# Kernel optimization log

Hardware: AMD Instinct MI355X
Metric: run time of the kernel (lower is better)

## Reference

```python
import jax, jax.numpy as jnp
import numpy as np

D_MODEL = 512
NUM_HEADS = 8


def setup_inputs() -> dict:
    key = jax.random.key(0)
    ks = jax.random.split(key, 12)
    B, S, D = 2, 4096, D_MODEL
    s = 1.0 / np.sqrt(D)
    return {
        "q": jax.random.normal(ks[0], (B, S, D), jnp.float32),
        "k": jax.random.normal(ks[1], (B, S, D), jnp.float32),
        "v": jax.random.normal(ks[2], (B, S, D), jnp.float32),
        "w_q": jax.random.normal(ks[3], (D, D), jnp.float32) * s,
        "b_q": jax.random.normal(ks[4], (D,), jnp.float32) * s,
        "w_k": jax.random.normal(ks[5], (D, D), jnp.float32) * s,
        "b_k": jax.random.normal(ks[6], (D,), jnp.float32) * s,
        "w_v": jax.random.normal(ks[7], (D, D), jnp.float32) * s,
        "b_v": jax.random.normal(ks[8], (D,), jnp.float32) * s,
        "w_o": jax.random.normal(ks[9], (D, D), jnp.float32) * s,
        "b_o": jax.random.normal(ks[10], (D,), jnp.float32) * s,
    }


def _split(x, num_heads):
    B, S, D = x.shape
    return x.reshape(B, S, num_heads, D // num_heads).transpose(0, 2, 1, 3)


def reference(q, k, v, w_q, b_q, w_k, b_k, w_v, b_v, w_o, b_o):
    # Linear projections (torch Linear: x @ W^T + b)
    qp = q @ w_q.T + b_q
    kp = k @ w_k.T + b_k
    vp = v @ w_v.T + b_v
    # split into heads: [B, H, S, d_head]
    qh = _split(qp, NUM_HEADS)
    kh = _split(kp, NUM_HEADS)
    vh = _split(vp, NUM_HEADS)
    d_head = qh.shape[-1]
    # NOTE: original scales by sqrt(d_model of the per-head tensor) == sqrt(d_head)
    score = jnp.einsum("bhqd,bhkd->bhqk", qh, kh) / jnp.sqrt(jnp.float32(d_head))
    attn = jax.nn.softmax(score, axis=-1)  # full [B,H,S,S] materialized, as in source
    out = jnp.einsum("bhqk,bhkd->bhqd", attn, vh)
    # concat heads back to [B, S, D]
    B, H, S, Dh = out.shape
    out = out.transpose(0, 2, 1, 3).reshape(B, S, H * Dh)
    return out @ w_o.T + b_o
```

## Files before the change

### kernel.cpp

```cpp
#include <hip/hip_runtime.h>
#include <math.h>

typedef __bf16 bf16_t;
typedef __bf16 bf16x4_v __attribute__((ext_vector_type(4)));
typedef __bf16 bf16x8_t __attribute__((ext_vector_type(8)));
typedef float f32x4_t __attribute__((ext_vector_type(4)));
typedef unsigned uint2_t __attribute__((ext_vector_type(2)));
typedef unsigned uint4_t __attribute__((ext_vector_type(4)));

#define S_LEN 4096
#define DM 512
#define NH 8
#define DH 64
#define MTOT 8192

#define Q_SCALE 0.1803368801111204f

#define REG   4194304
#define WREG  262144
#define W_OFF (3 * REG)
#define CVT_TOTAL (3 * REG + 4 * WREG)
#define QH_OFF CVT_TOTAL

__device__ inline f32x4_t mfma16(bf16x8_t a, bf16x8_t b, f32x4_t c) {
    return __builtin_amdgcn_mfma_f32_16x16x32_bf16(a, b, c, 0, 0, 0);
}

__device__ inline unsigned pkbf16(float a, float b) {
    unsigned short ra = __builtin_bit_cast(unsigned short, (bf16_t)a);
    unsigned short rb = __builtin_bit_cast(unsigned short, (bf16_t)b);
    return (unsigned)ra | ((unsigned)rb << 16);
}

__device__ inline void async_copy16(const void* g, void* l) {
    __builtin_amdgcn_global_load_lds(
        (const __attribute__((address_space(1))) void*)g,
        (__attribute__((address_space(3))) void*)l, 16, 0, 0);
}

__global__ __launch_bounds__(256) void cvt_all(
    const float* __restrict__ q, const float* __restrict__ k, const float* __restrict__ v,
    const float* __restrict__ wq, const float* __restrict__ wk,
    const float* __restrict__ wv, const float* __restrict__ wo,
    bf16_t* __restrict__ dst)
{
    long gidx = (long)blockIdx.x * 2048 + (long)threadIdx.x * 8;
    const float* src;
    long off = gidx;
    if      (gidx < 1L * REG)          { src = q; }
    else if (gidx < 2L * REG)          { src = k;  off = gidx - 1L * REG; }
    else if (gidx < 3L * REG)          { src = v;  off = gidx - 2L * REG; }
    else if (gidx < W_OFF + 1L * WREG) { src = wq; off = gidx - W_OFF; }
    else if (gidx < W_OFF + 2L * WREG) { src = wk; off = gidx - (W_OFF + 1L * WREG); }
    else if (gidx < W_OFF + 3L * WREG) { src = wv; off = gidx - (W_OFF + 2L * WREG); }
    else                               { src = wo; off = gidx - (W_OFF + 3L * WREG); }
    float4 a = *(const float4*)(src + off);
    float4 b = *(const float4*)(src + off + 4);
    bf16x8_t h;
    h[0] = (bf16_t)a.x; h[1] = (bf16_t)a.y; h[2] = (bf16_t)a.z; h[3] = (bf16_t)a.w;
    h[4] = (bf16_t)b.x; h[5] = (bf16_t)b.y; h[6] = (bf16_t)b.z; h[7] = (bf16_t)b.w;
    *(bf16x8_t*)(dst + gidx) = h;
}

__global__ __launch_bounds__(256) void gemm_qkv(
    const bf16_t* __restrict__ XWb,
    const float* __restrict__ B0, const float* __restrict__ B1, const float* __restrict__ B2,
    bf16_t* __restrict__ dst_base)
{
    const int p = blockIdx.z;
    const bf16_t* __restrict__ X = XWb + (size_t)p * REG;
    const bf16_t* __restrict__ W = XWb + W_OFF + (size_t)p * WREG;
    const float* __restrict__ Bi = (p == 0) ? B0 : ((p == 1) ? B1 : B2);
    bf16_t* __restrict__ dst = dst_base + (size_t)p * REG;

    const int m0 = blockIdx.x * 128;
    const int n0 = blockIdx.y * 128;
    const int tid = threadIdx.x;
    const int lane = tid & 63, wid = tid >> 6;
    const int lm = lane & 15, lg = lane >> 4;
    const int wm = (wid >> 1) * 64, wn = (wid & 1) * 64;

    __shared__ __align__(16) bf16_t As[128 * 64];
    __shared__ __align__(16) bf16_t Bs[128 * 64];

    f32x4_t acc[4][4] = {};

    const int r0 = tid >> 3, c7 = tid & 7;
    const int cA0 = ((lg) ^ (lm & 7)) * 8;
    const int cA1 = ((4 + lg) ^ (lm & 7)) * 8;

    for (int kb = 0; kb < DM / 64; ++kb) {
        const int k0 = kb * 64;
#pragma unroll
        for (int i = 0; i < 4; ++i) {
            int row = i * 32 + r0;
            int ch = c7 ^ (row & 7);
            async_copy16(X + (size_t)(m0 + row) * DM + k0 + ch * 8, (char*)As + (i * 256 + tid) * 16);
            async_copy16(W + (size_t)(n0 + row) * DM + k0 + ch * 8, (char*)Bs + (i * 256 + tid) * 16);
        }
        __syncthreads();
#pragma unroll
        for (int kd = 0; kd < 2; ++kd) {
            const int co = kd ? cA1 : cA0;
            bf16x8_t fa[4], fb[4];
#pragma unroll
            for (int mt = 0; mt < 4; ++mt) {
                fa[mt] = *(const bf16x8_t*)(As + (wm + mt * 16 + lm) * 64 + co);
                fb[mt] = *(const bf16x8_t*)(Bs + (wn + mt * 16 + lm) * 64 + co);
            }
            if (p < 2) {
#pragma unroll
                for (int mt = 0; mt < 4; ++mt)
#pragma unroll
                    for (int nt = 0; nt < 4; ++nt)
                        acc[nt][mt] = mfma16(fb[nt], fa[mt], acc[nt][mt]);
            } else {
#pragma unroll
                for (int mt = 0; mt < 4; ++mt)
#pragma unroll
                    for (int nt = 0; nt < 4; ++nt)
                        acc[mt][nt] = mfma16(fa[mt], fb[nt], acc[mt][nt]);
            }
        }
        __syncthreads();
    }

    if (p == 2) {
#pragma unroll
        for (int nt = 0; nt < 4; ++nt) {
            int col = n0 + wn + nt * 16 + lm;
            float bv = Bi[col];
            int h = (col >> 6) & 7, dc = col & 63;
#pragma unroll
            for (int mt = 0; mt < 4; ++mt) {
                int mrow = m0 + wm + mt * 16 + lg * 4;
                int bb = mrow >> 12, s = mrow & (S_LEN - 1);
                bf16x4_v pk;
#pragma unroll
                for (int r = 0; r < 4; ++r) pk[r] = (bf16_t)(acc[mt][nt][r] + bv);
                *(bf16x4_v*)&dst[(((size_t)(bb * NH + h)) * DH + dc) * S_LEN + s] = pk;
            }
        }
    } else {
        const float scale = (p == 0) ? Q_SCALE : 1.0f;
#pragma unroll
        for (int nt = 0; nt < 4; ++nt) {
            int ncol = n0 + wn + nt * 16 + lg * 4;
            float4 bv4 = *(const float4*)&Bi[ncol];
            int h = (ncol >> 6) & 7, dc = ncol & 63;
#pragma unroll
            for (int mt = 0; mt < 4; ++mt) {
                int m = m0 + wm + mt * 16 + lm;
                int bb = m >> 12, s = m & (S_LEN - 1);
                bf16x4_v pk;
                pk[0] = (bf16_t)((acc[nt][mt][0] + bv4.x) * scale);
                pk[1] = (bf16_t)((acc[nt][mt][1] + bv4.y) * scale);
                pk[2] = (bf16_t)((acc[nt][mt][2] + bv4.z) * scale);
                pk[3] = (bf16_t)((acc[nt][mt][3] + bv4.w) * scale);
                *(bf16x4_v*)&dst[(((size_t)(bb * NH + h)) * S_LEN + s) * DH + dc] = pk;
            }
        }
    }
}

__global__ __launch_bounds__(512, 4) void flash_attn(
    const bf16_t* __restrict__ Qh, const bf16_t* __restrict__ Kh,
    const bf16_t* __restrict__ Vth, bf16_t* __restrict__ O)
{
    const int bh = blockIdx.y;
    const int q0 = blockIdx.x * 128;
    const int tid = threadIdx.x;
    const int lane = tid & 63, wid = tid >> 6;
    const int lm = lane & 15, lg = lane >> 4;
    const int qg = wid & 3;
    const int kvh = wid >> 2;

    const bf16_t* __restrict__ Qb  = Qh  + (size_t)bh * S_LEN * DH;
    const bf16_t* __restrict__ Kb  = Kh  + (size_t)bh * S_LEN * DH;
    const bf16_t* __restrict__ Vtg = Vth + (size_t)bh * S_LEN * DH;

    __shared__ __align__(16) char smem[65536];

    bf16x8_t bQ[2][2];
#pragma unroll
    for (int nt = 0; nt < 2; ++nt)
#pragma unroll
        for (int kd = 0; kd < 2; ++kd)
            bQ[nt][kd] = *(const bf16x8_t*)(Qb + (size_t)(q0 + qg * 32 + nt * 16 + lm) * DH + kd * 32 + lg * 8);

    f32x4_t o_acc[4][2] = {};
    float l_acc[2] = {0.f, 0.f};

    const int srow = tid >> 3;
    const int slch = (tid & 7) ^ (srow & 7);
    const bf16_t* gK = Kb + (size_t)srow * DH + slch * 8;
    const bf16_t* gV = Vtg + (size_t)srow * S_LEN + slch * 8;

    const int cK0 = ((lg) ^ (lm & 7)) * 16;
    const int cK1 = ((4 + lg) ^ (lm & 7)) * 16;

    {
        char* b = smem;
        async_copy16(gK, b + tid * 16);
        async_copy16(gK + (size_t)64 * DH, b + 8192 + tid * 16);
        async_copy16(gV, b + 16384 + tid * 16);
        async_copy16(gV + 64, b + 24576 + tid * 16);
    }

    const int NT = S_LEN / 128;
    for (int it = 0; it < NT; ++it) {
        const char* buf = smem + (it & 1) * 32768;
        __syncthreads();

        if (it + 1 < NT) {
            char* nb = smem + ((it + 1) & 1) * 32768;
            const int kvb = (it + 1) * 128;
            async_copy16(gK + (size_t)kvb * DH, nb + tid * 16);
            async_copy16(gK + (size_t)(kvb + 64) * DH, nb + 8192 + tid * 16);
            async_copy16(gV + kvb, nb + 16384 + tid * 16);
            async_copy16(gV + kvb + 64, nb + 24576 + tid * 16);
        }

        const char* ksb = buf + kvh * 8192;
        const char* vsb = buf + 16384 + kvh * 8192;

        unsigned pk[4][2][2];
#pragma unroll
        for (int mt = 0; mt < 4; ++mt) {
            const char* krow = ksb + (mt * 16 + lm) * 128;
            bf16x8_t aK0 = *(const bf16x8_t*)(krow + cK0);
            bf16x8_t aK1 = *(const bf16x8_t*)(krow + cK1);
            f32x4_t s0 = {}, s1 = {};
            s0 = mfma16(aK0, bQ[0][0], s0);
            s0 = mfma16(aK1, bQ[0][1], s0);
            s1 = mfma16(aK0, bQ[1][0], s1);
            s1 = mfma16(aK1, bQ[1][1], s1);
            float e0 = __builtin_amdgcn_exp2f(s0[0]);
            float e1 = __builtin_amdgcn_exp2f(s0[1]);
            float e2 = __builtin_amdgcn_exp2f(s0[2]);
            float e3 = __builtin_amdgcn_exp2f(s0[3]);
            pk[mt][0][0] = pkbf16(e0, e1);
            pk[mt][0][1] = pkbf16(e2, e3);
            l_acc[0] += (e0 + e1) + (e2 + e3);
            float f0 = __builtin_amdgcn_exp2f(s1[0]);
            float f1 = __builtin_amdgcn_exp2f(s1[1]);
            float f2 = __builtin_amdgcn_exp2f(s1[2]);
            float f3 = __builtin_amdgcn_exp2f(s1[3]);
            pk[mt][1][0] = pkbf16(f0, f1);
            pk[mt][1][1] = pkbf16(f2, f3);
            l_acc[1] += (f0 + f1) + (f2 + f3);
        }

#pragma unroll
        for (int mt = 0; mt < 4; ++mt) {
            const char* vrow = vsb + (mt * 16 + lm) * 128;
#pragma unroll
            for (int cc = 0; cc < 2; ++cc) {
                const int ca = 2 * cc, cb = 2 * cc + 1;
                int pc0 = (ca * 2 + (lg >> 1)) ^ (lm & 7);
                int pc1 = (cb * 2 + (lg >> 1)) ^ (lm & 7);
                uint2_t va0 = *(const uint2_t*)(vrow + pc0 * 16 + (lg & 1) * 8);
                uint2_t va1 = *(const uint2_t*)(vrow + pc1 * 16 + (lg & 1) * 8);
                bf16x8_t vA = __builtin_bit_cast(bf16x8_t, (uint4_t){va0[0], va0[1], va1[0], va1[1]});
                bf16x8_t bP0 = __builtin_bit_cast(bf16x8_t, (uint4_t){pk[ca][0][0], pk[ca][0][1], pk[cb][0][0], pk[cb][0][1]});
                bf16x8_t bP1 = __builtin_bit_cast(bf16x8_t, (uint4_t){pk[ca][1][0], pk[ca][1][1], pk[cb][1][0], pk[cb][1][1]});
                o_acc[mt][0] = mfma16(vA, bP0, o_acc[mt][0]);
                o_acc[mt][1] = mfma16(vA, bP1, o_acc[mt][1]);
            }
        }
    }

#pragma unroll
    for (int nt = 0; nt < 2; ++nt) {
        l_acc[nt] += __shfl_xor(l_acc[nt], 16, 64);
        l_acc[nt] += __shfl_xor(l_acc[nt], 32, 64);
    }

    __syncthreads();

    float* ob = (float*)smem + qg * (32 * 66);
    float* lb = (float*)(smem + 33792);

    if (kvh == 1) {
#pragma unroll
        for (int nt = 0; nt < 2; ++nt) {
#pragma unroll
            for (int mt = 0; mt < 4; ++mt)
#pragma unroll
                for (int r = 0; r < 4; ++r)
                    ob[(nt * 16 + lm) * 66 + mt * 16 + lg * 4 + r] = o_acc[mt][nt][r];
            if (lg == 0) lb[qg * 32 + nt * 16 + lm] = l_acc[nt];
        }
    }
    __syncthreads();
    if (kvh == 0) {
        const int bb = bh >> 3, h = bh & 7;
#pragma unroll
        for (int nt = 0; nt < 2; ++nt) {
            float ltot = l_acc[nt] + lb[qg * 32 + nt * 16 + lm];
            float inv = 1.0f / ltot;
            int q = q0 + qg * 32 + nt * 16 + lm;
            size_t base = ((size_t)(bb * S_LEN + q)) * DM + h * DH;
#pragma unroll
            for (int mt = 0; mt < 4; ++mt) {
                const float* orow = &ob[(nt * 16 + lm) * 66 + mt * 16 + lg * 4];
                bf16x4_v pkd;
#pragma unroll
                for (int r = 0; r < 4; ++r)
                    pkd[r] = (bf16_t)((o_acc[mt][nt][r] + orow[r]) * inv);
                *(bf16x4_v*)&O[base + mt * 16 + lg * 4] = pkd;
            }
        }
    }
}

__global__ __launch_bounds__(256) void gemm_out(
    const bf16_t* __restrict__ A, const bf16_t* __restrict__ W,
    const float* __restrict__ Bi, float* __restrict__ out)
{
    const int m0 = blockIdx.x * 64;
    const int n0 = blockIdx.y * 128;
    const int tid = threadIdx.x;
    const int lane = tid & 63, wid = tid >> 6;
    const int lm = lane & 15, lg = lane >> 4;
    const int wm = (wid >> 1) * 32, wn = (wid & 1) * 64;

    __shared__ __align__(16) bf16_t As[64 * 64];
    __shared__ __align__(16) bf16_t Bs[128 * 64];

    f32x4_t acc[4][2] = {};

    const int r0 = tid >> 3, c7 = tid & 7;
    const int cA0 = ((lg) ^ (lm & 7)) * 8;
    const int cA1 = ((4 + lg) ^ (lm & 7)) * 8;

    for (int kb = 0; kb < DM / 64; ++kb) {
        const int k0 = kb * 64;
#pragma unroll
        for (int i = 0; i < 2; ++i) {
            int idx = i * 256 + tid;
            int row = idx >> 3;
            int ch = (idx & 7) ^ (row & 7);
            async_copy16(A + (size_t)(m0 + row) * DM + k0 + ch * 8, (char*)As + idx * 16);
        }
#pragma unroll
        for (int i = 0; i < 4; ++i) {
            int row = i * 32 + r0;
            int ch = c7 ^ (row & 7);
            async_copy16(W + (size_t)(n0 + row) * DM + k0 + ch * 8, (char*)Bs + (i * 256 + tid) * 16);
        }
        __syncthreads();
#pragma unroll
        for (int kd = 0; kd < 2; ++kd) {
            const int co = kd ? cA1 : cA0;
            bf16x8_t fa[2], fb[4];
#pragma unroll
            for (int mt = 0; mt < 2; ++mt)
                fa[mt] = *(const bf16x8_t*)(As + (wm + mt * 16 + lm) * 64 + co);
#pragma unroll
            for (int nt = 0; nt < 4; ++nt)
                fb[nt] = *(const bf16x8_t*)(Bs + (wn + nt * 16 + lm) * 64 + co);
#pragma unroll
            for (int nt = 0; nt < 4; ++nt)
#pragma unroll
                for (int mt = 0; mt < 2; ++mt)
                    acc[nt][mt] = mfma16(fb[nt], fa[mt], acc[nt][mt]);
        }
        __syncthreads();
    }

#pragma unroll
    for (int nt = 0; nt < 4; ++nt) {
        int ncol = n0 + wn + nt * 16 + lg * 4;
        float4 bv4 = *(const float4*)&Bi[ncol];
#pragma unroll
        for (int mt = 0; mt < 2; ++mt) {
            int m = m0 + wm + mt * 16 + lm;
            float4 ov;
            ov.x = acc[nt][mt][0] + bv4.x;
            ov.y = acc[nt][mt][1] + bv4.y;
            ov.z = acc[nt][mt][2] + bv4.z;
            ov.w = acc[nt][mt][3] + bv4.w;
            *(float4*)&out[(size_t)m * DM + ncol] = ov;
        }
    }
}

extern "C" void kernel_launch(void* const* d_in, const int* in_sizes, int n_in,
                              void* d_out, int out_size, void* d_ws, size_t ws_size,
                              hipStream_t stream)
{
    const float* q  = (const float*)d_in[0];
    const float* k  = (const float*)d_in[1];
    const float* v  = (const float*)d_in[2];
    const float* wq = (const float*)d_in[3];
    const float* bq = (const float*)d_in[4];
    const float* wk = (const float*)d_in[5];
    const float* bk = (const float*)d_in[6];
    const float* wv = (const float*)d_in[7];
    const float* bv = (const float*)d_in[8];
    const float* wo = (const float*)d_in[9];
    const float* bo = (const float*)d_in[10];
    float* out = (float*)d_out;

    bf16_t* ws = (bf16_t*)d_ws;
    bf16_t* XWb = ws;
    bf16_t* Qh  = ws + QH_OFF;
    bf16_t* Kh  = Qh + REG;
    bf16_t* VTh = Kh + REG;
    bf16_t* Ob  = ws;
    bf16_t* Wob = ws + W_OFF + 3 * (size_t)WREG;

    cvt_all<<<CVT_TOTAL / 2048, 256, 0, stream>>>(q, k, v, wq, wk, wv, wo, XWb);

    dim3 g1(MTOT / 128, DM / 128, 3);
    gemm_qkv<<<g1, 256, 0, stream>>>(XWb, bq, bk, bv, Qh);

    dim3 g2(S_LEN / 128, 2 * NH, 1);
    flash_attn<<<g2, 512, 0, stream>>>(Qh, Kh, VTh, Ob);

    dim3 g3(MTOT / 64, DM / 128, 1);
    gemm_out<<<g3, 256, 0, stream>>>(Ob, Wob, bo, out);
}
```

Before: 227.6 us.

## Fuse fp32-to-bf16 conversion into GEMMs and compute softmax row sums via MFMA

Drops the separate conversion kernel. The QKV and output GEMMs now load fp32 inputs and weights straight from global memory, convert them to bf16 in registers and store to LDS, with the X tile prefetched one k-step ahead. This removes a full fp32-read/bf16-write pass over the activations. In flash attention the per-row exp sums are now accumulated with an MFMA against a ones vector instead of scalar adds and shuffles, and the grid axes are swapped so consecutive blocks share the same M rows. The cost is synchronous global loads in the GEMM loops in place of async LDS copies, plus extra register pressure.

```diff
diff --git a/kernel.cpp b/kernel.cpp
--- a/kernel.cpp
+++ b/kernel.cpp
@@ -16,11 +16,7 @@
 
 #define Q_SCALE 0.1803368801111204f
 
-#define REG   4194304
-#define WREG  262144
-#define W_OFF (3 * REG)
-#define CVT_TOTAL (3 * REG + 4 * WREG)
-#define QH_OFF CVT_TOTAL
+#define REG 4194304
 
 __device__ inline f32x4_t mfma16(bf16x8_t a, bf16x8_t b, f32x4_t c) {
     return __builtin_amdgcn_mfma_f32_16x16x32_bf16(a, b, c, 0, 0, 0);
@@ -32,49 +28,33 @@
     return (unsigned)ra | ((unsigned)rb << 16);
 }
 
+__device__ inline bf16x8_t cvt8(float4 a, float4 b) {
+    bf16x8_t h;
+    h[0] = (bf16_t)a.x; h[1] = (bf16_t)a.y; h[2] = (bf16_t)a.z; h[3] = (bf16_t)a.w;
+    h[4] = (bf16_t)b.x; h[5] = (bf16_t)b.y; h[6] = (bf16_t)b.z; h[7] = (bf16_t)b.w;
+    return h;
+}
+
 __device__ inline void async_copy16(const void* g, void* l) {
     __builtin_amdgcn_global_load_lds(
         (const __attribute__((address_space(1))) void*)g,
         (__attribute__((address_space(3))) void*)l, 16, 0, 0);
 }
 
-__global__ __launch_bounds__(256) void cvt_all(
-    const float* __restrict__ q, const float* __restrict__ k, const float* __restrict__ v,
-    const float* __restrict__ wq, const float* __restrict__ wk,
-    const float* __restrict__ wv, const float* __restrict__ wo,
-    bf16_t* __restrict__ dst)
-{
-    long gidx = (long)blockIdx.x * 2048 + (long)threadIdx.x * 8;
-    const float* src;
-    long off = gidx;
-    if      (gidx < 1L * REG)          { src = q; }
-    else if (gidx < 2L * REG)          { src = k;  off = gidx - 1L * REG; }
-    else if (gidx < 3L * REG)          { src = v;  off = gidx - 2L * REG; }
-    else if (gidx < W_OFF + 1L * WREG) { src = wq; off = gidx - W_OFF; }
-    else if (gidx < W_OFF + 2L * WREG) { src = wk; off = gidx - (W_OFF + 1L * WREG); }
-    else if (gidx < W_OFF + 3L * WREG) { src = wv; off = gidx - (W_OFF + 2L * WREG); }
-    else                               { src = wo; off = gidx - (W_OFF + 3L * WREG); }
-    float4 a = *(const float4*)(src + off);
-    float4 b = *(const float4*)(src + off + 4);
-    bf16x8_t h;
-    h[0] = (bf16_t)a.x; h[1] = (bf16_t)a.y; h[2] = (bf16_t)a.z; h[3] = (bf16_t)a.w;
-    h[4] = (bf16_t)b.x; h[5] = (bf16_t)b.y; h[6] = (bf16_t)b.z; h[7] = (bf16_t)b.w;
-    *(bf16x8_t*)(dst + gidx) = h;
-}
-
 __global__ __launch_bounds__(256) void gemm_qkv(
-    const bf16_t* __restrict__ XWb,
+    const float* __restrict__ X0, const float* __restrict__ X1, const float* __restrict__ X2,
+    const float* __restrict__ W0, const float* __restrict__ W1, const float* __restrict__ W2,
     const float* __restrict__ B0, const float* __restrict__ B1, const float* __restrict__ B2,
     bf16_t* __restrict__ dst_base)
 {
     const int p = blockIdx.z;
-    const bf16_t* __restrict__ X = XWb + (size_t)p * REG;
-    const bf16_t* __restrict__ W = XWb + W_OFF + (size_t)p * WREG;
+    const float* __restrict__ X  = (p == 0) ? X0 : ((p == 1) ? X1 : X2);
+    const float* __restrict__ W  = (p == 0) ? W0 : ((p == 1) ? W1 : W2);
     const float* __restrict__ Bi = (p == 0) ? B0 : ((p == 1) ? B1 : B2);
     bf16_t* __restrict__ dst = dst_base + (size_t)p * REG;
 
-    const int m0 = blockIdx.x * 128;
-    const int n0 = blockIdx.y * 128;
+    const int n0 = blockIdx.x * 128;
+    const int m0 = blockIdx.y * 128;
     const int tid = threadIdx.x;
     const int lane = tid & 63, wid = tid >> 6;
     const int lm = lane & 15, lg = lane >> 4;
@@ -89,16 +69,39 @@
     const int cA0 = ((lg) ^ (lm & 7)) * 8;
     const int cA1 = ((4 + lg) ^ (lm & 7)) * 8;
 
+    int rows[4], chs[4];
+#pragma unroll
+    for (int i = 0; i < 4; ++i) { rows[i] = i * 32 + r0; chs[i] = c7 ^ (rows[i] & 7); }
+
+    float4 pa0[4], pa1[4];
+#pragma unroll
+    for (int i = 0; i < 4; ++i) {
+        const float* s = X + (size_t)(m0 + rows[i]) * DM + chs[i] * 8;
+        pa0[i] = *(const float4*)s; pa1[i] = *(const float4*)(s + 4);
+    }
+
     for (int kb = 0; kb < DM / 64; ++kb) {
-        const int k0 = kb * 64;
+        float4 pb0[4], pb1[4];
 #pragma unroll
         for (int i = 0; i < 4; ++i) {
-            int row = i * 32 + r0;
-            int ch = c7 ^ (row & 7);
-            async_copy16(X + (size_t)(m0 + row) * DM + k0 + ch * 8, (char*)As + (i * 256 + tid) * 16);
-            async_copy16(W + (size_t)(n0 + row) * DM + k0 + ch * 8, (char*)Bs + (i * 256 + tid) * 16);
+            const float* s = W + (size_t)(n0 + rows[i]) * DM + kb * 64 + chs[i] * 8;
+            pb0[i] = *(const float4*)s; pb1[i] = *(const float4*)(s + 4);
         }
         __syncthreads();
+#pragma unroll
+        for (int i = 0; i < 4; ++i) {
+            *(bf16x8_t*)((char*)As + (i * 256 + tid) * 16) = cvt8(pa0[i], pa1[i]);
+            *(bf16x8_t*)((char*)Bs + (i * 256 + tid) * 16) = cvt8(pb0[i], pb1[i]);
+        }
+        __syncthreads();
+        if (kb < DM / 64 - 1) {
+            const int k1 = (kb + 1) * 64;
+#pragma unroll
+            for (int i = 0; i < 4; ++i) {
+                const float* s = X + (size_t)(m0 + rows[i]) * DM + k1 + chs[i] * 8;
+                pa0[i] = *(const float4*)s; pa1[i] = *(const float4*)(s + 4);
+            }
+        }
 #pragma unroll
         for (int kd = 0; kd < 2; ++kd) {
             const int co = kd ? cA1 : cA0;
@@ -122,7 +125,6 @@
                         acc[mt][nt] = mfma16(fa[mt], fb[nt], acc[mt][nt]);
             }
         }
-        __syncthreads();
     }
 
     if (p == 2) {
@@ -188,8 +190,12 @@
         for (int kd = 0; kd < 2; ++kd)
             bQ[nt][kd] = *(const bf16x8_t*)(Qb + (size_t)(q0 + qg * 32 + nt * 16 + lm) * DH + kd * 32 + lg * 8);
 
+    bf16x8_t onesA;
+#pragma unroll
+    for (int i = 0; i < 8; ++i) onesA[i] = (bf16_t)1.0f;
+
     f32x4_t o_acc[4][2] = {};
-    float l_acc[2] = {0.f, 0.f};
+    f32x4_t acc_l[2] = {};
 
     const int srow = tid >> 3;
     const int slch = (tid & 7) ^ (srow & 7);
@@ -235,47 +241,33 @@
             s0 = mfma16(aK1, bQ[0][1], s0);
             s1 = mfma16(aK0, bQ[1][0], s1);
             s1 = mfma16(aK1, bQ[1][1], s1);
-            float e0 = __builtin_amdgcn_exp2f(s0[0]);
-            float e1 = __builtin_amdgcn_exp2f(s0[1]);
-            float e2 = __builtin_amdgcn_exp2f(s0[2]);
-            float e3 = __builtin_amdgcn_exp2f(s0[3]);
-            pk[mt][0][0] = pkbf16(e0, e1);
-            pk[mt][0][1] = pkbf16(e2, e3);
-            l_acc[0] += (e0 + e1) + (e2 + e3);
-            float f0 = __builtin_amdgcn_exp2f(s1[0]);
-            float f1 = __builtin_amdgcn_exp2f(s1[1]);
-            float f2 = __builtin_amdgcn_exp2f(s1[2]);
-            float f3 = __builtin_amdgcn_exp2f(s1[3]);
-            pk[mt][1][0] = pkbf16(f0, f1);
-            pk[mt][1][1] = pkbf16(f2, f3);
-            l_acc[1] += (f0 + f1) + (f2 + f3);
-        }
-
-#pragma unroll
-        for (int mt = 0; mt < 4; ++mt) {
-            const char* vrow = vsb + (mt * 16 + lm) * 128;
-#pragma unroll
-            for (int cc = 0; cc < 2; ++cc) {
-                const int ca = 2 * cc, cb = 2 * cc + 1;
-                int pc0 = (ca * 2 + (lg >> 1)) ^ (lm & 7);
-                int pc1 = (cb * 2 + (lg >> 1)) ^ (lm & 7);
+            pk[mt][0][0] = pkbf16(__builtin_amdgcn_exp2f(s0[0]), __builtin_amdgcn_exp2f(s0[1]));
+            pk[mt][0][1] = pkbf16(__builtin_amdgcn_exp2f(s0[2]), __builtin_amdgcn_exp2f(s0[3]));
+            pk[mt][1][0] = pkbf16(__builtin_amdgcn_exp2f(s1[0]), __builtin_amdgcn_exp2f(s1[1]));
+            pk[mt][1][1] = pkbf16(__builtin_amdgcn_exp2f(s1[2]), __builtin_amdgcn_exp2f(s1[3]));
+        }
+
+#pragma unroll
+        for (int cc = 0; cc < 2; ++cc) {
+            const int ca = 2 * cc, cb = 2 * cc + 1;
+            bf16x8_t bP0 = __builtin_bit_cast(bf16x8_t, (uint4_t){pk[ca][0][0], pk[ca][0][1], pk[cb][0][0], pk[cb][0][1]});
+            bf16x8_t bP1 = __builtin_bit_cast(bf16x8_t, (uint4_t){pk[ca][1][0], pk[ca][1][1], pk[cb][1][0], pk[cb][1][1]});
+            acc_l[0] = mfma16(onesA, bP0, acc_l[0]);
+            acc_l[1] = mfma16(onesA, bP1, acc_l[1]);
+            const int pc0 = (ca * 2 + (lg >> 1)) ^ (lm & 7);
+            const int pc1 = (cb * 2 + (lg >> 1)) ^ (lm & 7);
+#pragma unroll
+            for (int mt = 0; mt < 4; ++mt) {
+                const char* vrow = vsb + (mt * 16 + lm) * 128;
                 uint2_t va0 = *(const uint2_t*)(vrow + pc0 * 16 + (lg & 1) * 8);
                 uint2_t va1 = *(const uint2_t*)(vrow + pc1 * 16 + (lg & 1) * 8);
                 bf16x8_t vA = __builtin_bit_cast(bf16x8_t, (uint4_t){va0[0], va0[1], va1[0], va1[1]});
-                bf16x8_t bP0 = __builtin_bit_cast(bf16x8_t, (uint4_t){pk[ca][0][0], pk[ca][0][1], pk[cb][0][0], pk[cb][0][1]});
-                bf16x8_t bP1 = __builtin_bit_cast(bf16x8_t, (uint4_t){pk[ca][1][0], pk[ca][1][1], pk[cb][1][0], pk[cb][1][1]});
                 o_acc[mt][0] = mfma16(vA, bP0, o_acc[mt][0]);
                 o_acc[mt][1] = mfma16(vA, bP1, o_acc[mt][1]);
             }
         }
     }
 
-#pragma unroll
-    for (int nt = 0; nt < 2; ++nt) {
-        l_acc[nt] += __shfl_xor(l_acc[nt], 16, 64);
-        l_acc[nt] += __shfl_xor(l_acc[nt], 32, 64);
-    }
-
     __syncthreads();
 
     float* ob = (float*)smem + qg * (32 * 66);
@@ -289,7 +281,7 @@
 #pragma unroll
                 for (int r = 0; r < 4; ++r)
                     ob[(nt * 16 + lm) * 66 + mt * 16 + lg * 4 + r] = o_acc[mt][nt][r];
-            if (lg == 0) lb[qg * 32 + nt * 16 + lm] = l_acc[nt];
+            if (lg == 0) lb[qg * 32 + nt * 16 + lm] = acc_l[nt][0];
         }
     }
     __syncthreads();
@@ -297,7 +289,7 @@
         const int bb = bh >> 3, h = bh & 7;
 #pragma unroll
         for (int nt = 0; nt < 2; ++nt) {
-            float ltot = l_acc[nt] + lb[qg * 32 + nt * 16 + lm];
+            float ltot = acc_l[nt][0] + lb[qg * 32 + nt * 16 + lm];
             float inv = 1.0f / ltot;
             int q = q0 + qg * 32 + nt * 16 + lm;
             size_t base = ((size_t)(bb * S_LEN + q)) * DM + h * DH;
@@ -315,11 +307,11 @@
 }
 
 __global__ __launch_bounds__(256) void gemm_out(
-    const bf16_t* __restrict__ A, const bf16_t* __restrict__ W,
+    const bf16_t* __restrict__ A, const float* __restrict__ W,
     const float* __restrict__ Bi, float* __restrict__ out)
 {
-    const int m0 = blockIdx.x * 64;
-    const int n0 = blockIdx.y * 128;
+    const int n0 = blockIdx.x * 128;
+    const int m0 = blockIdx.y * 64;
     const int tid = threadIdx.x;
     const int lane = tid & 63, wid = tid >> 6;
     const int lm = lane & 15, lg = lane >> 4;
@@ -334,21 +326,31 @@
     const int cA0 = ((lg) ^ (lm & 7)) * 8;
     const int cA1 = ((4 + lg) ^ (lm & 7)) * 8;
 
+    int arow[2], ach[2], brow[4], bch[4];
+#pragma unroll
+    for (int i = 0; i < 2; ++i) {
+        int idx = i * 256 + tid;
+        arow[i] = idx >> 3; ach[i] = (idx & 7) ^ (arow[i] & 7);
+    }
+#pragma unroll
+    for (int i = 0; i < 4; ++i) { brow[i] = i * 32 + r0; bch[i] = c7 ^ (brow[i] & 7); }
+
     for (int kb = 0; kb < DM / 64; ++kb) {
         const int k0 = kb * 64;
-#pragma unroll
-        for (int i = 0; i < 2; ++i) {
-            int idx = i * 256 + tid;
-            int row = idx >> 3;
-            int ch = (idx & 7) ^ (row & 7);
-            async_copy16(A + (size_t)(m0 + row) * DM + k0 + ch * 8, (char*)As + idx * 16);
-        }
+        float4 pb0[4], pb1[4];
 #pragma unroll
         for (int i = 0; i < 4; ++i) {
-            int row = i * 32 + r0;
-            int ch = c7 ^ (row & 7);
-            async_copy16(W + (size_t)(n0 + row) * DM + k0 + ch * 8, (char*)Bs + (i * 256 + tid) * 16);
-        }
+            const float* s = W + (size_t)(n0 + brow[i]) * DM + k0 + bch[i] * 8;
+            pb0[i] = *(const float4*)s; pb1[i] = *(const float4*)(s + 4);
+        }
+        __syncthreads();
+#pragma unroll
+        for (int i = 0; i < 2; ++i)
+            async_copy16(A + (size_t)(m0 + arow[i]) * DM + k0 + ach[i] * 8,
+                         (char*)As + (i * 256 + tid) * 16);
+#pragma unroll
+        for (int i = 0; i < 4; ++i)
+            *(bf16x8_t*)((char*)Bs + (i * 256 + tid) * 16) = cvt8(pb0[i], pb1[i]);
         __syncthreads();
 #pragma unroll
         for (int kd = 0; kd < 2; ++kd) {
@@ -366,7 +368,6 @@
                 for (int mt = 0; mt < 2; ++mt)
                     acc[nt][mt] = mfma16(fb[nt], fa[mt], acc[nt][mt]);
         }
-        __syncthreads();
     }
 
 #pragma unroll
@@ -403,22 +404,18 @@
     const float* bo = (const float*)d_in[10];
     float* out = (float*)d_out;
 
-    bf16_t* ws = (bf16_t*)d_ws;
-    bf16_t* XWb = ws;
-    bf16_t* Qh  = ws + QH_OFF;
-    bf16_t* Kh  = Qh + REG;
-    bf16_t* VTh = Kh + REG;
+    bf16_t* ws  = (bf16_t*)d_ws;
     bf16_t* Ob  = ws;
-    bf16_t* Wob = ws + W_OFF + 3 * (size_t)WREG;
-
-    cvt_all<<<CVT_TOTAL / 2048, 256, 0, stream>>>(q, k, v, wq, wk, wv, wo, XWb);
-
-    dim3 g1(MTOT / 128, DM / 128, 3);
-    gemm_qkv<<<g1, 256, 0, stream>>>(XWb, bq, bk, bv, Qh);
+    bf16_t* Qh  = ws + REG;
+    bf16_t* Kh  = ws + 2 * (size_t)REG;
+    bf16_t* VTh = ws + 3 * (size_t)REG;
+
+    dim3 g1(DM / 128, MTOT / 128, 3);
+    gemm_qkv<<<g1, 256, 0, stream>>>(q, k, v, wq, wk, wv, bq, bk, bv, Qh);
 
     dim3 g2(S_LEN / 128, 2 * NH, 1);
     flash_attn<<<g2, 512, 0, stream>>>(Qh, Kh, VTh, Ob);
 
-    dim3 g3(MTOT / 64, DM / 128, 1);
-    gemm_out<<<g3, 256, 0, stream>>>(Ob, Wob, bo, out);
-}
+    dim3 g3(DM / 128, MTOT / 64, 1);
+    gemm_out<<<g3, 256, 0, stream>>>(Ob, wo, bo, out);
+}
```

Measured after the change: 231.5 us. No clear change (+1.7%).
